# Performance work log

Hardware: AMD Instinct MI355X
Metric: run time of the kernel (lower is better)

## Reference

```python
import jax, jax.numpy as jnp
import numpy as np

EPS = 1e-5
DN = ('NCHW', 'OIHW', 'NCHW')

def _conv(x, w, b):
    y = jax.lax.conv_general_dilated(x, w, (1, 1), 'SAME', dimension_numbers=DN)
    return y + b.reshape(1, -1, 1, 1)

def _bn(x, g, bt, m, v):
    # inference-mode BatchNorm2d
    scale = g * jax.lax.rsqrt(v + EPS)
    return (x - m.reshape(1, -1, 1, 1)) * scale.reshape(1, -1, 1, 1) + bt.reshape(1, -1, 1, 1)


def setup_inputs() -> dict:
    key = jax.random.key(0)
    ks = jax.random.split(key, 12)
    B, C, H, W = 32, 1, 1024, 1024
    inp = {
        'x':  jax.random.normal(ks[0], (B, C, H, W), jnp.float32),
        # conv3x3_bn_r (shared module, used 3 times)
        'wa': jax.random.normal(ks[1], (1, 1, 3, 3), jnp.float32) * 0.2,
        'ba': jnp.zeros((1,), jnp.float32),
        'ga': jnp.ones((1,), jnp.float32),
        'bta': jnp.zeros((1,), jnp.float32),
        'ma': jax.random.normal(ks[2], (1,), jnp.float32) * 0.1,
        'va': jax.random.uniform(ks[3], (1,), jnp.float32) + 0.5,
        # conv3x3_bn
        'wb': jax.random.normal(ks[4], (1, 1, 3, 3), jnp.float32) * 0.2,
        'bb': jnp.zeros((1,), jnp.float32),
        'gb': jnp.ones((1,), jnp.float32),
        'btb': jnp.zeros((1,), jnp.float32),
        'mb': jax.random.normal(ks[5], (1,), jnp.float32) * 0.1,
        'vb': jax.random.uniform(ks[6], (1,), jnp.float32) + 0.5,
        # conv1x1_bn
        'wc': jax.random.normal(ks[7], (1, 1, 1, 1), jnp.float32) * 0.2,
        'bc': jnp.zeros((1,), jnp.float32),
        'gc': jnp.ones((1,), jnp.float32),
        'btc': jnp.zeros((1,), jnp.float32),
        'mc': jax.random.normal(ks[8], (1,), jnp.float32) * 0.1,
        'vc': jax.random.uniform(ks[9], (1,), jnp.float32) + 0.5,
        # conv3x3_r
        'wd': jax.random.normal(ks[10], (1, 1, 3, 3), jnp.float32) * 0.2,
        'bd': jnp.zeros((1,), jnp.float32),
        # conv1x1
        'we': jax.random.normal(ks[11], (1, 1, 1, 1), jnp.float32) * 0.2,
        'be': jnp.zeros((1,), jnp.float32),
    }
    return inp


def reference(x, wa, ba, ga, bta, ma, va, wb, bb, gb, btb, mb, vb,
              wc, bc, gc, btc, mc, vc, wd, bd, we, be):
    # t = 0 (top-left corner): right->left cummax + bottom->up cummax
    # conv3x3_bn_r is one shared module; x1 == x2 in the original.
    x1 = jax.nn.relu(_bn(_conv(x, wa, ba), ga, bta, ma, va))
    i1 = jax.lax.cummax(x1, axis=3, reverse=True)  # RightLeftMaxPooling
    i2 = jax.lax.cummax(x1, axis=2, reverse=True)  # DownUpMaxPooling
    b1 = _bn(_conv(i1 + i2, wb, bb), gb, btb, mb, vb)
    b2 = _bn(_conv(x, wc, bc), gc, btc, mc, vc)
    s = jax.nn.relu(b1 + b2)
    out = jax.nn.relu(_bn(_conv(s, wa, ba), ga, bta, ma, va))  # shared conv3x3_bn_r again
    out = jax.nn.relu(_conv(out, wd, bd))
    out = _conv(out, we, be)
    return out
```

## Files before the change

### kernel.cpp

```cpp
#include <hip/hip_runtime.h>
#include <math.h>

#define EPS 1e-5f
constexpr int IMG_H = 1024;
constexpr int IMG_W = 1024;
constexpr int NIMG  = 32;

__device__ __forceinline__ float frelu(float v) { return fmaxf(v, 0.f); }

struct Row { float4 q[4]; };

__device__ __forceinline__ void load_row(const float* __restrict__ xim, int gr,
                                         int lane, Row& R)
{
    if ((unsigned)gr < (unsigned)IMG_H) {
        const float4* rp = (const float4*)(xim + (size_t)gr * IMG_W);
#pragma unroll
        for (int q = 0; q < 4; ++q) R.q[q] = rp[lane + 64 * q];
    } else {
#pragma unroll
        for (int q = 0; q < 4; ++q) R.q[q] = make_float4(0.f, 0.f, 0.f, 0.f);
    }
}

__device__ __forceinline__ void conv3_row(const Row& Ra, const Row& Rb, const Row& Rc,
                                          const float* ws, float bias, int lane,
                                          float4* v)
{
    const Row* rows[3] = { &Ra, &Rb, &Rc };
#pragma unroll
    for (int q = 0; q < 4; ++q) {
        float acc0 = bias, acc1 = bias, acc2 = bias, acc3 = bias;
#pragma unroll
        for (int dy = 0; dy < 3; ++dy) {
            float4 C = rows[dy]->q[q];
            float Lw = __shfl_up(C.w, 1, 64);
            float Bq = 0.f;
            if (q > 0) Bq = __shfl(rows[dy]->q[q - 1].w, 63, 64);
            if (lane == 0) Lw = Bq;
            float Rx = __shfl_down(C.x, 1, 64);
            float Aq = 0.f;
            if (q < 3) Aq = __shfl(rows[dy]->q[q + 1].x, 0, 64);
            if (lane == 63) Rx = Aq;
            const float w0 = ws[3 * dy], w1 = ws[3 * dy + 1], w2 = ws[3 * dy + 2];
            acc0 += w0 * Lw  + w1 * C.x + w2 * C.y;
            acc1 += w0 * C.x + w1 * C.y + w2 * C.z;
            acc2 += w0 * C.y + w1 * C.z + w2 * C.w;
            acc3 += w0 * C.z + w1 * C.w + w2 * Rx;
        }
        v[q] = make_float4(frelu(acc0), frelu(acc1), frelu(acc2), frelu(acc3));
    }
}

__global__ __launch_bounds__(256) void k_rowstats(
    const float* __restrict__ x,
    const float* __restrict__ wa, const float* __restrict__ ba,
    const float* __restrict__ ga, const float* __restrict__ bta,
    const float* __restrict__ ma, const float* __restrict__ va,
    float* __restrict__ M8, float* __restrict__ I1S)
{
    const int bid  = blockIdx.x;
    const int img  = bid >> 6;
    const int b16  = bid & 63;
    const int lane = threadIdx.x & 63;
    const int wv   = threadIdx.x >> 6;
    const int rb   = b16 * 16 + wv * 4;

    const float scale = ga[0] * rsqrtf(va[0] + EPS);
    float w_s[9];
#pragma unroll
    for (int k = 0; k < 9; ++k) w_s[k] = wa[k] * scale;
    const float bias = (ba[0] - ma[0]) * scale + bta[0];

    const float* xim = x + (size_t)img * IMG_H * IMG_W;

    Row A, B, C;
    load_row(xim, rb - 1, lane, A);
    load_row(xim, rb,     lane, B);

    float4 cm[4];
#pragma unroll
    for (int q = 0; q < 4; ++q) cm[q] = make_float4(0.f, 0.f, 0.f, 0.f);

#pragma unroll
    for (int rr = 0; rr < 4; ++rr) {
        const int r = rb + rr;
        load_row(xim, r + 1, lane, C);
        float4 v[4];
        conv3_row(A, B, C, w_s, bias, lane, v);

        float4 s[4]; float T4[4], e[4];
#pragma unroll
        for (int q = 0; q < 4; ++q) {
            float s3 = v[q].w;
            float s2 = fmaxf(v[q].z, s3);
            float s1 = fmaxf(v[q].y, s2);
            float s0 = fmaxf(v[q].x, s1);
            s[q] = make_float4(s0, s1, s2, s3);
            float mm = s0;
#pragma unroll
            for (int off = 1; off < 64; off <<= 1) {
                float o = __shfl_down(mm, off, 64);
                if (lane + off < 64) mm = fmaxf(mm, o);
            }
            T4[q] = __shfl(mm, 0, 64);
            float ex = __shfl_down(mm, 1, 64);
            if (lane == 63) ex = -INFINITY;
            e[q] = ex;
        }
        float Rr[4];
        Rr[3] = -INFINITY;
        Rr[2] = T4[3];
        Rr[1] = fmaxf(T4[2], Rr[2]);
        Rr[0] = fmaxf(T4[1], Rr[1]);

        if ((lane & 15) == 0) {
#pragma unroll
            for (int q = 0; q < 4; ++q) {
                const float ee  = fmaxf(e[q], Rr[q]);
                const float i1w = fmaxf(s[q].w, ee);
                I1S[((size_t)img * IMG_H + r) * 16 + (q * 4 + (lane >> 4))] = i1w;
            }
        }
#pragma unroll
        for (int q = 0; q < 4; ++q) {
            cm[q].x = fmaxf(cm[q].x, v[q].x); cm[q].y = fmaxf(cm[q].y, v[q].y);
            cm[q].z = fmaxf(cm[q].z, v[q].z); cm[q].w = fmaxf(cm[q].w, v[q].w);
        }
        A = B; B = C;
    }

    __shared__ float4 wcm[4][256];
#pragma unroll
    for (int q = 0; q < 4; ++q) wcm[wv][64 * q + lane] = cm[q];
    __syncthreads();

    const int tid = threadIdx.x;
    float4 a0 = wcm[0][tid], a1 = wcm[1][tid];
    float4 a2 = wcm[2][tid], a3 = wcm[3][tid];
    float4 f0 = make_float4(fmaxf(a0.x, a1.x), fmaxf(a0.y, a1.y),
                            fmaxf(a0.z, a1.z), fmaxf(a0.w, a1.w));
    float4 f1 = make_float4(fmaxf(a2.x, a3.x), fmaxf(a2.y, a3.y),
                            fmaxf(a2.z, a3.z), fmaxf(a2.w, a3.w));
    const int s0 = b16 * 2;
    ((float4*)(M8 + ((size_t)img * 128 + s0) * IMG_W))[tid]     = f0;
    ((float4*)(M8 + ((size_t)img * 128 + s0 + 1) * IMG_W))[tid] = f1;
}

__global__ __launch_bounds__(256) void k_seed(
    const float* __restrict__ M8, float* __restrict__ I2S)
{
    const int gid = blockIdx.x * 256 + threadIdx.x;
    const int img = gid >> 10;
    const int c   = gid & 1023;
    const float* mp = M8  + (size_t)img * 128 * IMG_W + c;
    float*       ip = I2S + (size_t)img * 16  * IMG_W + c;

    float run = 0.f;
#pragma unroll 8
    for (int s = 127; s >= 8; --s) {
        if ((s & 7) == 0) ip[(size_t)(s / 8 - 1) * IMG_W] = run;
        run = fmaxf(run, mp[(size_t)s * IMG_W]);
    }
}

__global__ __launch_bounds__(256) void k_tile(
    const float* __restrict__ x,
    const float* __restrict__ I1S, const float* __restrict__ I2S,
    const float* __restrict__ wa, const float* __restrict__ ba,
    const float* __restrict__ ga, const float* __restrict__ bta,
    const float* __restrict__ ma, const float* __restrict__ va,
    const float* __restrict__ wb, const float* __restrict__ bb,
    const float* __restrict__ gb, const float* __restrict__ btb,
    const float* __restrict__ mb, const float* __restrict__ vb,
    const float* __restrict__ wc, const float* __restrict__ bc,
    const float* __restrict__ gcp, const float* __restrict__ btc,
    const float* __restrict__ mc, const float* __restrict__ vc,
    const float* __restrict__ wd, const float* __restrict__ bd,
    const float* __restrict__ we, const float* __restrict__ be,
    float* __restrict__ out)
{
    __shared__ float B1[75 * 72];
    __shared__ float B2[70 * 72];

    const int bid = blockIdx.x;
    const int img = bid >> 8;
    const int tr  = (bid >> 4) & 15;
    const int tc  = bid & 15;
    const int r0  = tr * 64, c0 = tc * 64;
    const int tid = threadIdx.x;
    const int k0  = tc + 1;
    const int m1  = tr;

    const float sa = ga[0] * rsqrtf(va[0] + EPS);
    float was[9];
#pragma unroll
    for (int k = 0; k < 9; ++k) was[k] = wa[k] * sa;
    const float biasa = (ba[0] - ma[0]) * sa + bta[0];

    const float sb = gb[0] * rsqrtf(vb[0] + EPS);
    float wbs[9];
#pragma unroll
    for (int k = 0; k < 9; ++k) wbs[k] = wb[k] * sb;
    const float biasb = (bb[0] - mb[0]) * sb + btb[0];

    const float sc = gcp[0] * rsqrtf(vc[0] + EPS);
    const float kc = wc[0] * sc;
    const float biasc = (bc[0] - mc[0]) * sc + btc[0];

    float wd9[9];
#pragma unroll
    for (int k = 0; k < 9; ++k) wd9[k] = wd[k];
    const float bd0 = bd[0], we0 = we[0], be0 = be[0];

    const float* xim = x + (size_t)img * IMG_H * IMG_W;

#pragma unroll
    for (int it = 0; it < 2; ++it) {
        const int m = tid + 256 * it;
        if (m < 270) {
            const int mi = m / 18, mj = m - mi * 18;
            const int wr0 = mi * 5, wc0 = mj * 4;
            const int gr0 = r0 + wr0 - 4;
            const int gc0 = c0 + wc0 - 4;
            const bool fastC = (gc0 >= 0) && (gc0 + 5 < IMG_W);
            float w[7][6];
#pragma unroll
            for (int rr = 0; rr < 7; ++rr) {
                const int gr = gr0 + rr;
                if ((unsigned)gr < (unsigned)IMG_H) {
                    const float* rp = xim + (size_t)gr * IMG_W;
                    if (fastC) {
                        float4 a4 = *(const float4*)(rp + gc0);
                        float2 b2 = *(const float2*)(rp + gc0 + 4);
                        w[rr][0] = a4.x; w[rr][1] = a4.y; w[rr][2] = a4.z;
                        w[rr][3] = a4.w; w[rr][4] = b2.x; w[rr][5] = b2.y;
                    } else {
#pragma unroll
                        for (int j = 0; j < 6; ++j) {
                            const int gc = gc0 + j;
                            w[rr][j] = ((unsigned)gc < (unsigned)IMG_W) ? rp[gc] : 0.f;
                        }
                    }
                } else {
#pragma unroll
                    for (int j = 0; j < 6; ++j) w[rr][j] = 0.f;
                }
            }
#pragma unroll
            for (int rr = 0; rr < 5; ++rr) {
                const int grx = r0 - 3 + wr0 + rr;
                float res4[4];
#pragma unroll
                for (int cc = 0; cc < 4; ++cc) {
                    float acc = biasa;
#pragma unroll
                    for (int dy = 0; dy < 3; ++dy)
#pragma unroll
                        for (int dx = 0; dx < 3; ++dx)
                            acc += was[3 * dy + dx] * w[rr + dy][cc + dx];
                    const int gcx = c0 - 3 + wc0 + cc;
                    float val = 0.f;
                    if ((unsigned)grx < (unsigned)IMG_H && (unsigned)gcx < (unsigned)IMG_W)
                        val = frelu(acc);
                    res4[cc] = val;
                }
                *(float4*)&B1[(wr0 + rr) * 72 + wc0] =
                    make_float4(res4[0], res4[1], res4[2], res4[3]);
            }
        }
    }
    __syncthreads();

    {
        const int wv = tid >> 6, lane = tid & 63;
#pragma unroll
        for (int k = 0; k < 18; ++k) {
            const int wr = k * 4 + wv;
            if (wr < 70) {
                const int row = r0 - 3 + wr;
                float seed = 0.f;
                if (k0 < 16 && (unsigned)row < (unsigned)IMG_H)
                    seed = I1S[((size_t)img * IMG_H + row) * 16 + k0];
                const float lo = B1[wr * 72 + lane];
                const float hi = (lane < 6) ? B1[wr * 72 + 64 + lane] : 0.f;
                float sh = hi;
#pragma unroll
                for (int off = 1; off < 64; off <<= 1) {
                    float o = __shfl_down(sh, off, 64);
                    if (lane + off < 64) sh = fmaxf(sh, o);
                }
                sh = fmaxf(sh, seed);
                const float hi_all = __shfl(sh, 0, 64);
                float sl = lo;
#pragma unroll
                for (int off = 1; off < 64; off <<= 1) {
                    float o = __shfl_down(sl, off, 64);
                    if (lane + off < 64) sl = fmaxf(sl, o);
                }
                B2[wr * 72 + lane] = fmaxf(sl, hi_all);
                if (lane < 6) B2[wr * 72 + 64 + lane] = sh;
            }
        }
    }
    __syncthreads();

    if (tid < 70) {
        const int col = c0 - 3 + tid;
        const bool colIn = (unsigned)col < (unsigned)IMG_W;
        float run = 0.f;
        if (m1 < 15 && colIn) run = I2S[((size_t)img * 16 + m1) * IMG_W + col];
#pragma unroll
        for (int wr = 74; wr >= 70; --wr) run = fmaxf(run, B1[wr * 72 + tid]);
#pragma unroll 7
        for (int wr = 69; wr >= 0; --wr) {
            run = fmaxf(run, B1[wr * 72 + tid]);
            const int r = r0 - 3 + wr;
            const bool inb = colIn && ((unsigned)r < (unsigned)IMG_H);
            const float tv = B2[wr * 72 + tid] + run;
            B2[wr * 72 + tid] = inb ? tv : 0.f;
        }
    }
    __syncthreads();

#pragma unroll
    for (int it = 0; it < 2; ++it) {
        const int m = tid + 256 * it;
        if (m < 289) {
            const int mi = m / 17, mj = m - mi * 17;
            const int si0 = mi * 4, sj0 = mj * 4;
            float win[6][6];
#pragma unroll
            for (int r = 0; r < 6; ++r) {
                const float* p = &B2[(si0 + r) * 72 + sj0];
                float4 a4 = *(const float4*)p;
                float2 b2 = *(const float2*)(p + 4);
                win[r][0] = a4.x; win[r][1] = a4.y; win[r][2] = a4.z;
                win[r][3] = a4.w; win[r][4] = b2.x; win[r][5] = b2.y;
            }
#pragma unroll
            for (int a = 0; a < 4; ++a) {
                float res4[4];
#pragma unroll
                for (int b = 0; b < 4; ++b) {
                    float acc = biasb;
#pragma unroll
                    for (int dy = 0; dy < 3; ++dy)
#pragma unroll
                        for (int dx = 0; dx < 3; ++dx)
                            acc += wbs[3 * dy + dx] * win[a + dy][b + dx];
                    const int gr = r0 - 2 + si0 + a, gc = c0 - 2 + sj0 + b;
                    float sres = 0.f;
                    if ((unsigned)gr < (unsigned)IMG_H && (unsigned)gc < (unsigned)IMG_W) {
                        const float xv = xim[(size_t)gr * IMG_W + gc];
                        sres = frelu(acc + xv * kc + biasc);
                    }
                    res4[b] = sres;
                }
                *(float4*)&B1[(si0 + a) * 72 + sj0] =
                    make_float4(res4[0], res4[1], res4[2], res4[3]);
            }
        }
    }
    __syncthreads();

#pragma unroll
    for (int it = 0; it < 2; ++it) {
        const int m = tid + 256 * it;
        if (m < 289) {
            const int mi = m / 17, mj = m - mi * 17;
            const int ai0 = mi * 4, aj0 = mj * 4;
            float win[6][6];
#pragma unroll
            for (int r = 0; r < 6; ++r) {
                const float* p = &B1[(ai0 + r) * 72 + aj0];
                float4 a4 = *(const float4*)p;
                float2 b2 = *(const float2*)(p + 4);
                win[r][0] = a4.x; win[r][1] = a4.y; win[r][2] = a4.z;
                win[r][3] = a4.w; win[r][4] = b2.x; win[r][5] = b2.y;
            }
#pragma unroll
            for (int a = 0; a < 4; ++a) {
                float res4[4];
#pragma unroll
                for (int b = 0; b < 4; ++b) {
                    float acc = biasa;
#pragma unroll
                    for (int dy = 0; dy < 3; ++dy)
#pragma unroll
                        for (int dx = 0; dx < 3; ++dx)
                            acc += was[3 * dy + dx] * win[a + dy][b + dx];
                    const int gr = r0 - 1 + ai0 + a, gc = c0 - 1 + aj0 + b;
                    float r1 = 0.f;
                    if ((unsigned)gr < (unsigned)IMG_H && (unsigned)gc < (unsigned)IMG_W)
                        r1 = frelu(acc);
                    res4[b] = r1;
                }
                *(float4*)&B2[(ai0 + a) * 72 + aj0] =
                    make_float4(res4[0], res4[1], res4[2], res4[3]);
            }
        }
    }
    __syncthreads();

    {
        const int oi0 = (tid >> 4) << 2, oj0 = (tid & 15) << 2;
        float win[6][6];
#pragma unroll
        for (int r = 0; r < 6; ++r) {
            const float* p = &B2[(oi0 + r) * 72 + oj0];
            float4 a4 = *(const float4*)p;
            float2 b2 = *(const float2*)(p + 4);
            win[r][0] = a4.x; win[r][1] = a4.y; win[r][2] = a4.z;
            win[r][3] = a4.w; win[r][4] = b2.x; win[r][5] = b2.y;
        }
        float* oim = out + (size_t)img * IMG_H * IMG_W;
#pragma unroll
        for (int a = 0; a < 4; ++a) {
            float res4[4];
#pragma unroll
            for (int b = 0; b < 4; ++b) {
                float acc = bd0;
#pragma unroll
                for (int dy = 0; dy < 3; ++dy)
#pragma unroll
                    for (int dx = 0; dx < 3; ++dx)
                        acc += wd9[3 * dy + dx] * win[a + dy][b + dx];
                res4[b] = frelu(acc) * we0 + be0;
            }
            *(float4*)&oim[(size_t)(r0 + oi0 + a) * IMG_W + (c0 + oj0)] =
                make_float4(res4[0], res4[1], res4[2], res4[3]);
        }
    }
}

extern "C" void kernel_launch(void* const* d_in, const int* in_sizes, int n_in,
                              void* d_out, int out_size, void* d_ws, size_t ws_size,
                              hipStream_t stream)
{
    const float* x   = (const float*)d_in[0];
    const float* wa  = (const float*)d_in[1];
    const float* ba  = (const float*)d_in[2];
    const float* ga  = (const float*)d_in[3];
    const float* bta = (const float*)d_in[4];
    const float* ma  = (const float*)d_in[5];
    const float* va  = (const float*)d_in[6];
    const float* wb  = (const float*)d_in[7];
    const float* bb  = (const float*)d_in[8];
    const float* gb  = (const float*)d_in[9];
    const float* btb = (const float*)d_in[10];
    const float* mb  = (const float*)d_in[11];
    const float* vb  = (const float*)d_in[12];
    const float* wc  = (const float*)d_in[13];
    const float* bc  = (const float*)d_in[14];
    const float* gcp = (const float*)d_in[15];
    const float* btc = (const float*)d_in[16];
    const float* mc  = (const float*)d_in[17];
    const float* vc  = (const float*)d_in[18];
    const float* wd  = (const float*)d_in[19];
    const float* bd  = (const float*)d_in[20];
    const float* we  = (const float*)d_in[21];
    const float* be  = (const float*)d_in[22];

    float* outp = (float*)d_out;
    float* M8   = (float*)d_ws;
    float* I1S  = M8 + (size_t)NIMG * 128 * IMG_W;
    float* I2S  = I1S + (size_t)NIMG * IMG_H * 16;

    k_rowstats<<<dim3(NIMG * 64), dim3(256), 0, stream>>>(
        x, wa, ba, ga, bta, ma, va, M8, I1S);
    k_seed<<<dim3(128), dim3(256), 0, stream>>>(M8, I2S);
    k_tile<<<dim3(NIMG * 256), dim3(256), 0, stream>>>(
        x, I1S, I2S, wa, ba, ga, bta, ma, va, wb, bb, gb, btb, mb, vb,
        wc, bc, gcp, btc, mc, vc, wd, bd, we, be, outp);
}
```

Baseline: 576.1 us.

## Shrink tile halo, restructure seeds and scans across front and tile kernels

The main tile kernel drops from 64x64 tiles with a 5-row bottom halo to 64x32 tiles with a smaller halo. Seeds are made finer: I1S now holds 32 column seeds per row and I2S is built from M8 plus new partial maxima (M8part). The front kernel processes 2 rows per wave in 8-row strips instead of 4 rows per wave, so it launches twice as many blocks. The column cummax in the tile becomes a per-wave partial max followed by a merged row loop, replacing the separate single-wave scan pass. This trims redundant halo convolution and LDS traffic and raises occupancy, at the cost of more blocks, more seed traffic and more halo overhead relative to the narrower tile width.

Result: faster. 511.9 us (-11.1%).

```diff
diff --git a/kernel.cpp b/kernel.cpp
--- a/kernel.cpp
+++ b/kernel.cpp
@@ -8,63 +8,19 @@
 
 __device__ __forceinline__ float frelu(float v) { return fmaxf(v, 0.f); }
 
-struct Row { float4 q[4]; };
-
-__device__ __forceinline__ void load_row(const float* __restrict__ xim, int gr,
-                                         int lane, Row& R)
-{
-    if ((unsigned)gr < (unsigned)IMG_H) {
-        const float4* rp = (const float4*)(xim + (size_t)gr * IMG_W);
-#pragma unroll
-        for (int q = 0; q < 4; ++q) R.q[q] = rp[lane + 64 * q];
-    } else {
-#pragma unroll
-        for (int q = 0; q < 4; ++q) R.q[q] = make_float4(0.f, 0.f, 0.f, 0.f);
-    }
-}
-
-__device__ __forceinline__ void conv3_row(const Row& Ra, const Row& Rb, const Row& Rc,
-                                          const float* ws, float bias, int lane,
-                                          float4* v)
-{
-    const Row* rows[3] = { &Ra, &Rb, &Rc };
-#pragma unroll
-    for (int q = 0; q < 4; ++q) {
-        float acc0 = bias, acc1 = bias, acc2 = bias, acc3 = bias;
-#pragma unroll
-        for (int dy = 0; dy < 3; ++dy) {
-            float4 C = rows[dy]->q[q];
-            float Lw = __shfl_up(C.w, 1, 64);
-            float Bq = 0.f;
-            if (q > 0) Bq = __shfl(rows[dy]->q[q - 1].w, 63, 64);
-            if (lane == 0) Lw = Bq;
-            float Rx = __shfl_down(C.x, 1, 64);
-            float Aq = 0.f;
-            if (q < 3) Aq = __shfl(rows[dy]->q[q + 1].x, 0, 64);
-            if (lane == 63) Rx = Aq;
-            const float w0 = ws[3 * dy], w1 = ws[3 * dy + 1], w2 = ws[3 * dy + 2];
-            acc0 += w0 * Lw  + w1 * C.x + w2 * C.y;
-            acc1 += w0 * C.x + w1 * C.y + w2 * C.z;
-            acc2 += w0 * C.y + w1 * C.z + w2 * C.w;
-            acc3 += w0 * C.z + w1 * C.w + w2 * Rx;
-        }
-        v[q] = make_float4(frelu(acc0), frelu(acc1), frelu(acc2), frelu(acc3));
-    }
-}
-
-__global__ __launch_bounds__(256) void k_rowstats(
+__global__ __launch_bounds__(256) void k_front(
     const float* __restrict__ x,
     const float* __restrict__ wa, const float* __restrict__ ba,
     const float* __restrict__ ga, const float* __restrict__ bta,
     const float* __restrict__ ma, const float* __restrict__ va,
-    float* __restrict__ M8, float* __restrict__ I1S)
+    float* __restrict__ M8, float* __restrict__ M8part, float* __restrict__ I1S)
 {
-    const int bid  = blockIdx.x;
-    const int img  = bid >> 6;
-    const int b16  = bid & 63;
-    const int lane = threadIdx.x & 63;
-    const int wv   = threadIdx.x >> 6;
-    const int rb   = b16 * 16 + wv * 4;
+    const int bid   = blockIdx.x;
+    const int img   = bid >> 7;
+    const int strip = bid & 127;
+    const int lane  = threadIdx.x & 63;
+    const int wv    = threadIdx.x >> 6;
+    const int rb    = strip * 8 + wv * 2;
 
     const float scale = ga[0] * rsqrtf(va[0] + EPS);
     float w_s[9];
@@ -74,29 +30,55 @@
 
     const float* xim = x + (size_t)img * IMG_H * IMG_W;
 
-    Row A, B, C;
-    load_row(xim, rb - 1, lane, A);
-    load_row(xim, rb,     lane, B);
-
-    float4 cm[4];
-#pragma unroll
-    for (int q = 0; q < 4; ++q) cm[q] = make_float4(0.f, 0.f, 0.f, 0.f);
-
-#pragma unroll
-    for (int rr = 0; rr < 4; ++rr) {
-        const int r = rb + rr;
-        load_row(xim, r + 1, lane, C);
+    float4 X[4][4];
+#pragma unroll
+    for (int ri = 0; ri < 4; ++ri) {
+        const int gr = rb - 1 + ri;
+        if (gr >= 0 && gr < IMG_H) {
+            const float4* rp = (const float4*)(xim + (size_t)gr * IMG_W);
+#pragma unroll
+            for (int q = 0; q < 4; ++q) X[ri][q] = rp[lane + 64 * q];
+        } else {
+#pragma unroll
+            for (int q = 0; q < 4; ++q) X[ri][q] = make_float4(0.f, 0.f, 0.f, 0.f);
+        }
+    }
+
+    float4 wm[4], w1r1[4];
+#pragma unroll
+    for (int rr = 0; rr < 2; ++rr) {
         float4 v[4];
-        conv3_row(A, B, C, w_s, bias, lane, v);
-
-        float4 s[4]; float T4[4], e[4];
+#pragma unroll
+        for (int q = 0; q < 4; ++q) {
+            float acc0 = bias, acc1 = bias, acc2 = bias, acc3 = bias;
+#pragma unroll
+            for (int dy = 0; dy < 3; ++dy) {
+                float4 C = X[rr + dy][q];
+                float Lw = __shfl_up(C.w, 1, 64);
+                float Bq = 0.f;
+                if (q > 0) Bq = __shfl(X[rr + dy][q - 1].w, 63, 64);
+                if (lane == 0) Lw = Bq;
+                float Rx = __shfl_down(C.x, 1, 64);
+                float Aq = 0.f;
+                if (q < 3) Aq = __shfl(X[rr + dy][q + 1].x, 0, 64);
+                if (lane == 63) Rx = Aq;
+                const float w0 = w_s[3 * dy], w1 = w_s[3 * dy + 1], w2 = w_s[3 * dy + 2];
+                acc0 += w0 * Lw  + w1 * C.x + w2 * C.y;
+                acc1 += w0 * C.x + w1 * C.y + w2 * C.z;
+                acc2 += w0 * C.y + w1 * C.z + w2 * C.w;
+                acc3 += w0 * C.z + w1 * C.w + w2 * Rx;
+            }
+            v[q] = make_float4(frelu(acc0), frelu(acc1), frelu(acc2), frelu(acc3));
+        }
+
+        float sW[4], T4[4], e[4];
 #pragma unroll
         for (int q = 0; q < 4; ++q) {
             float s3 = v[q].w;
             float s2 = fmaxf(v[q].z, s3);
             float s1 = fmaxf(v[q].y, s2);
             float s0 = fmaxf(v[q].x, s1);
-            s[q] = make_float4(s0, s1, s2, s3);
+            sW[q] = s3;
             float mm = s0;
 #pragma unroll
             for (int off = 1; off < 64; off <<= 1) {
@@ -114,57 +96,81 @@
         Rr[1] = fmaxf(T4[2], Rr[2]);
         Rr[0] = fmaxf(T4[1], Rr[1]);
 
-        if ((lane & 15) == 0) {
+        if ((lane & 7) == 0) {
+            const int r = rb + rr;
 #pragma unroll
             for (int q = 0; q < 4; ++q) {
-                const float ee  = fmaxf(e[q], Rr[q]);
-                const float i1w = fmaxf(s[q].w, ee);
-                I1S[((size_t)img * IMG_H + r) * 16 + (q * 4 + (lane >> 4))] = i1w;
-            }
-        }
-#pragma unroll
-        for (int q = 0; q < 4; ++q) {
-            cm[q].x = fmaxf(cm[q].x, v[q].x); cm[q].y = fmaxf(cm[q].y, v[q].y);
-            cm[q].z = fmaxf(cm[q].z, v[q].z); cm[q].w = fmaxf(cm[q].w, v[q].w);
-        }
-        A = B; B = C;
-    }
-
-    __shared__ float4 wcm[4][256];
-#pragma unroll
-    for (int q = 0; q < 4; ++q) wcm[wv][64 * q + lane] = cm[q];
+                const float val = fmaxf(sW[q], fmaxf(e[q], Rr[q]));
+                I1S[((size_t)img * IMG_H + r) * 32 + (q * 8 + (lane >> 3))] = val;
+            }
+        }
+
+        if (rr == 0) {
+#pragma unroll
+            for (int q = 0; q < 4; ++q) wm[q] = v[q];
+        } else {
+#pragma unroll
+            for (int q = 0; q < 4; ++q) {
+                wm[q].x = fmaxf(wm[q].x, v[q].x); wm[q].y = fmaxf(wm[q].y, v[q].y);
+                wm[q].z = fmaxf(wm[q].z, v[q].z); wm[q].w = fmaxf(wm[q].w, v[q].w);
+            }
+#pragma unroll
+            for (int q = 0; q < 4; ++q) w1r1[q] = v[q];
+        }
+    }
+
+    __shared__ float4 wmax[5][256];
+#pragma unroll
+    for (int q = 0; q < 4; ++q) wmax[wv][64 * q + lane] = wm[q];
+    if (wv == 1) {
+#pragma unroll
+        for (int q = 0; q < 4; ++q) wmax[4][64 * q + lane] = w1r1[q];
+    }
     __syncthreads();
 
     const int tid = threadIdx.x;
-    float4 a0 = wcm[0][tid], a1 = wcm[1][tid];
-    float4 a2 = wcm[2][tid], a3 = wcm[3][tid];
-    float4 f0 = make_float4(fmaxf(a0.x, a1.x), fmaxf(a0.y, a1.y),
-                            fmaxf(a0.z, a1.z), fmaxf(a0.w, a1.w));
-    float4 f1 = make_float4(fmaxf(a2.x, a3.x), fmaxf(a2.y, a3.y),
-                            fmaxf(a2.z, a3.z), fmaxf(a2.w, a3.w));
-    const int s0 = b16 * 2;
-    ((float4*)(M8 + ((size_t)img * 128 + s0) * IMG_W))[tid]     = f0;
-    ((float4*)(M8 + ((size_t)img * 128 + s0 + 1) * IMG_W))[tid] = f1;
+    float4 a0 = wmax[0][tid], a1 = wmax[1][tid], a2 = wmax[2][tid], a3 = wmax[3][tid];
+    float4 f;
+    f.x = fmaxf(fmaxf(a0.x, a1.x), fmaxf(a2.x, a3.x));
+    f.y = fmaxf(fmaxf(a0.y, a1.y), fmaxf(a2.y, a3.y));
+    f.z = fmaxf(fmaxf(a0.z, a1.z), fmaxf(a2.z, a3.z));
+    f.w = fmaxf(fmaxf(a0.w, a1.w), fmaxf(a2.w, a3.w));
+    ((float4*)(M8 + ((size_t)img * 128 + strip) * IMG_W))[tid] = f;
+
+    if (strip >= 8 && (strip & 7) == 0) {
+        float4 r3v = wmax[4][tid];
+        float4 fp;
+        fp.x = fmaxf(r3v.x, fmaxf(a2.x, a3.x));
+        fp.y = fmaxf(r3v.y, fmaxf(a2.y, a3.y));
+        fp.z = fmaxf(r3v.z, fmaxf(a2.z, a3.z));
+        fp.w = fmaxf(r3v.w, fmaxf(a2.w, a3.w));
+        ((float4*)(M8part + ((size_t)img * 15 + ((strip >> 3) - 1)) * IMG_W))[tid] = fp;
+    }
 }
 
-__global__ __launch_bounds__(256) void k_seed(
-    const float* __restrict__ M8, float* __restrict__ I2S)
+__global__ __launch_bounds__(256) void k_seed2(
+    const float* __restrict__ M8, const float* __restrict__ M8part,
+    float* __restrict__ I2S)
 {
     const int gid = blockIdx.x * 256 + threadIdx.x;
     const int img = gid >> 10;
     const int c   = gid & 1023;
-    const float* mp = M8  + (size_t)img * 128 * IMG_W + c;
-    float*       ip = I2S + (size_t)img * 16  * IMG_W + c;
+    const float* mp = M8 + (size_t)img * 128 * IMG_W + c;
 
     float run = 0.f;
-#pragma unroll 8
-    for (int s = 127; s >= 8; --s) {
-        if ((s & 7) == 0) ip[(size_t)(s / 8 - 1) * IMG_W] = run;
+#pragma unroll 7
+    for (int s = 127; s >= 9; --s) {
         run = fmaxf(run, mp[(size_t)s * IMG_W]);
+        if ((s & 7) == 1) {
+            const int m = (s - 9) >> 3;
+            const size_t o = ((size_t)img * 15 + m) * IMG_W + c;
+            I2S[o] = fmaxf(run, M8part[o]);
+        }
     }
 }
 
-__global__ __launch_bounds__(256) void k_tile(
+#define PITCH 44
+__global__ __launch_bounds__(256, 6) void k_tile(
     const float* __restrict__ x,
     const float* __restrict__ I1S, const float* __restrict__ I2S,
     const float* __restrict__ wa, const float* __restrict__ ba,
@@ -180,17 +186,35 @@
     const float* __restrict__ we, const float* __restrict__ be,
     float* __restrict__ out)
 {
-    __shared__ float B1[75 * 72];
-    __shared__ float B2[70 * 72];
+    __shared__ float B1[70 * PITCH];
+    __shared__ float B2[68 * PITCH];
+    __shared__ float P[4][PITCH];
 
     const int bid = blockIdx.x;
-    const int img = bid >> 8;
-    const int tr  = (bid >> 4) & 15;
-    const int tc  = bid & 15;
-    const int r0  = tr * 64, c0 = tc * 64;
+    const int img = bid >> 9;
+    const int tr  = (bid >> 5) & 15;
+    const int tc  = bid & 31;
+    const int r0  = tr * 64, c0 = tc * 32;
     const int tid = threadIdx.x;
-    const int k0  = tc + 1;
-    const int m1  = tr;
+    const int lane = tid & 63;
+    const int wv   = tid >> 6;
+
+    const float* xim = x + (size_t)img * IMG_H * IMG_W;
+
+    float i2sv = 0.f;
+    if (tr < 15 && lane < 38) {
+        const int col = c0 - 3 + lane;
+        if ((unsigned)col < (unsigned)IMG_W)
+            i2sv = I2S[((size_t)img * 15 + tr) * IMG_W + col];
+    }
+    const int g0 = wv * 18;
+    const int nrows = (wv == 3) ? 16 : 18;
+    float seed1v = 0.f;
+    if (lane < nrows && tc < 31) {
+        const int row = r0 - 3 + g0 + lane;
+        if ((unsigned)row < (unsigned)IMG_H)
+            seed1v = I1S[((size_t)img * IMG_H + row) * 32 + (tc + 1)];
+    }
 
     const float sa = ga[0] * rsqrtf(va[0] + EPS);
     float was[9];
@@ -213,42 +237,38 @@
     for (int k = 0; k < 9; ++k) wd9[k] = wd[k];
     const float bd0 = bd[0], we0 = we[0], be0 = be[0];
 
-    const float* xim = x + (size_t)img * IMG_H * IMG_W;
-
-#pragma unroll
-    for (int it = 0; it < 2; ++it) {
-        const int m = tid + 256 * it;
-        if (m < 270) {
-            const int mi = m / 18, mj = m - mi * 18;
-            const int wr0 = mi * 5, wc0 = mj * 4;
-            const int gr0 = r0 + wr0 - 4;
-            const int gc0 = c0 + wc0 - 4;
-            const bool fastC = (gc0 >= 0) && (gc0 + 5 < IMG_W);
-            float w[7][6];
-#pragma unroll
-            for (int rr = 0; rr < 7; ++rr) {
-                const int gr = gr0 + rr;
-                if ((unsigned)gr < (unsigned)IMG_H) {
-                    const float* rp = xim + (size_t)gr * IMG_W;
-                    if (fastC) {
-                        float4 a4 = *(const float4*)(rp + gc0);
-                        float2 b2 = *(const float2*)(rp + gc0 + 4);
-                        w[rr][0] = a4.x; w[rr][1] = a4.y; w[rr][2] = a4.z;
-                        w[rr][3] = a4.w; w[rr][4] = b2.x; w[rr][5] = b2.y;
-                    } else {
-#pragma unroll
-                        for (int j = 0; j < 6; ++j) {
-                            const int gc = gc0 + j;
-                            w[rr][j] = ((unsigned)gc < (unsigned)IMG_W) ? rp[gc] : 0.f;
-                        }
+    if (tid < 180) {
+        const int mi = tid / 10, mj = tid - mi * 10;
+        const int wr0 = mi * 4, wc0 = mj * 4;
+        const int gr0 = r0 - 4 + wr0;
+        const int gc0 = c0 - 4 + wc0;
+        const bool fastC = (gc0 >= 0) && (gc0 + 5 < IMG_W);
+        float w[6][6];
+#pragma unroll
+        for (int rr = 0; rr < 6; ++rr) {
+            const int gr = gr0 + rr;
+            if ((unsigned)gr < (unsigned)IMG_H) {
+                const float* rp = xim + (size_t)gr * IMG_W;
+                if (fastC) {
+                    float4 a4 = *(const float4*)(rp + gc0);
+                    float2 b2 = *(const float2*)(rp + gc0 + 4);
+                    w[rr][0] = a4.x; w[rr][1] = a4.y; w[rr][2] = a4.z;
+                    w[rr][3] = a4.w; w[rr][4] = b2.x; w[rr][5] = b2.y;
+                } else {
+#pragma unroll
+                    for (int j = 0; j < 6; ++j) {
+                        const int gc = gc0 + j;
+                        w[rr][j] = ((unsigned)gc < (unsigned)IMG_W) ? rp[gc] : 0.f;
                     }
-                } else {
-#pragma unroll
-                    for (int j = 0; j < 6; ++j) w[rr][j] = 0.f;
                 }
-            }
-#pragma unroll
-            for (int rr = 0; rr < 5; ++rr) {
+            } else {
+#pragma unroll
+                for (int j = 0; j < 6; ++j) w[rr][j] = 0.f;
+            }
+        }
+#pragma unroll
+        for (int rr = 0; rr < 4; ++rr) {
+            if (wr0 + rr < 70) {
                 const int grx = r0 - 3 + wr0 + rr;
                 float res4[4];
 #pragma unroll
@@ -265,7 +285,7 @@
                         val = frelu(acc);
                     res4[cc] = val;
                 }
-                *(float4*)&B1[(wr0 + rr) * 72 + wc0] =
+                *(float4*)&B1[(wr0 + rr) * PITCH + wc0] =
                     make_float4(res4[0], res4[1], res4[2], res4[3]);
             }
         }
@@ -273,114 +293,99 @@
     __syncthreads();
 
     {
-        const int wv = tid >> 6, lane = tid & 63;
-#pragma unroll
+        float pm = 0.f;
+        if (lane < 38) {
+            for (int k = 0; k < nrows; ++k)
+                pm = fmaxf(pm, B1[(g0 + k) * PITCH + lane]);
+            P[wv][lane] = pm;
+        }
+    }
+    __syncthreads();
+
+    {
+        float run = i2sv;
+#pragma unroll
+        for (int w2 = 1; w2 < 4; ++w2)
+            if (w2 > wv && lane < 38) run = fmaxf(run, P[w2][lane]);
+#pragma unroll 6
         for (int k = 0; k < 18; ++k) {
-            const int wr = k * 4 + wv;
-            if (wr < 70) {
+            if (k < nrows) {
+                const int lr = nrows - 1 - k;
+                const int wr = g0 + lr;
+                const float xv = (lane < 38) ? B1[wr * PITCH + lane] : 0.f;
+                float mm = xv;
+#pragma unroll
+                for (int off = 1; off < 64; off <<= 1) {
+                    float o = __shfl_down(mm, off, 64);
+                    if (lane + off < 64) mm = fmaxf(mm, o);
+                }
+                const float sd = __shfl(seed1v, lr, 64);
+                const float i1v = fmaxf(mm, sd);
+                run = fmaxf(run, xv);
                 const int row = r0 - 3 + wr;
-                float seed = 0.f;
-                if (k0 < 16 && (unsigned)row < (unsigned)IMG_H)
-                    seed = I1S[((size_t)img * IMG_H + row) * 16 + k0];
-                const float lo = B1[wr * 72 + lane];
-                const float hi = (lane < 6) ? B1[wr * 72 + 64 + lane] : 0.f;
-                float sh = hi;
-#pragma unroll
-                for (int off = 1; off < 64; off <<= 1) {
-                    float o = __shfl_down(sh, off, 64);
-                    if (lane + off < 64) sh = fmaxf(sh, o);
+                const int col = c0 - 3 + lane;
+                const bool inb = ((unsigned)row < (unsigned)IMG_H) &&
+                                 ((unsigned)col < (unsigned)IMG_W);
+                if (lane < 38)
+                    B1[wr * PITCH + lane] = inb ? (i1v + run) : 0.f;
+            }
+        }
+    }
+    __syncthreads();
+
+    if (tid < 153) {
+        const int mi = tid / 9, mj = tid - mi * 9;
+        const int si0 = mi * 4, sj0 = mj * 4;
+        float win[6][6];
+#pragma unroll
+        for (int r = 0; r < 6; ++r) {
+            const float* p = &B1[(si0 + r) * PITCH + sj0];
+            float4 a4 = *(const float4*)p;
+            float2 b2 = *(const float2*)(p + 4);
+            win[r][0] = a4.x; win[r][1] = a4.y; win[r][2] = a4.z;
+            win[r][3] = a4.w; win[r][4] = b2.x; win[r][5] = b2.y;
+        }
+#pragma unroll
+        for (int a = 0; a < 4; ++a) {
+            float res4[4];
+#pragma unroll
+            for (int b = 0; b < 4; ++b) {
+                float acc = biasb;
+#pragma unroll
+                for (int dy = 0; dy < 3; ++dy)
+#pragma unroll
+                    for (int dx = 0; dx < 3; ++dx)
+                        acc += wbs[3 * dy + dx] * win[a + dy][b + dx];
+                const int gr = r0 - 2 + si0 + a, gc = c0 - 2 + sj0 + b;
+                float sres = 0.f;
+                if ((unsigned)gr < (unsigned)IMG_H && (unsigned)gc < (unsigned)IMG_W) {
+                    const float xv = xim[(size_t)gr * IMG_W + gc];
+                    sres = frelu(acc + xv * kc + biasc);
                 }
-                sh = fmaxf(sh, seed);
-                const float hi_all = __shfl(sh, 0, 64);
-                float sl = lo;
-#pragma unroll
-                for (int off = 1; off < 64; off <<= 1) {
-                    float o = __shfl_down(sl, off, 64);
-                    if (lane + off < 64) sl = fmaxf(sl, o);
-                }
-                B2[wr * 72 + lane] = fmaxf(sl, hi_all);
-                if (lane < 6) B2[wr * 72 + 64 + lane] = sh;
-            }
-        }
-    }
-    __syncthreads();
-
-    if (tid < 70) {
-        const int col = c0 - 3 + tid;
-        const bool colIn = (unsigned)col < (unsigned)IMG_W;
-        float run = 0.f;
-        if (m1 < 15 && colIn) run = I2S[((size_t)img * 16 + m1) * IMG_W + col];
-#pragma unroll
-        for (int wr = 74; wr >= 70; --wr) run = fmaxf(run, B1[wr * 72 + tid]);
-#pragma unroll 7
-        for (int wr = 69; wr >= 0; --wr) {
-            run = fmaxf(run, B1[wr * 72 + tid]);
-            const int r = r0 - 3 + wr;
-            const bool inb = colIn && ((unsigned)r < (unsigned)IMG_H);
-            const float tv = B2[wr * 72 + tid] + run;
-            B2[wr * 72 + tid] = inb ? tv : 0.f;
-        }
-    }
-    __syncthreads();
-
-#pragma unroll
-    for (int it = 0; it < 2; ++it) {
-        const int m = tid + 256 * it;
-        if (m < 289) {
-            const int mi = m / 17, mj = m - mi * 17;
-            const int si0 = mi * 4, sj0 = mj * 4;
-            float win[6][6];
-#pragma unroll
-            for (int r = 0; r < 6; ++r) {
-                const float* p = &B2[(si0 + r) * 72 + sj0];
-                float4 a4 = *(const float4*)p;
-                float2 b2 = *(const float2*)(p + 4);
-                win[r][0] = a4.x; win[r][1] = a4.y; win[r][2] = a4.z;
-                win[r][3] = a4.w; win[r][4] = b2.x; win[r][5] = b2.y;
-            }
-#pragma unroll
-            for (int a = 0; a < 4; ++a) {
-                float res4[4];
-#pragma unroll
-                for (int b = 0; b < 4; ++b) {
-                    float acc = biasb;
-#pragma unroll
-                    for (int dy = 0; dy < 3; ++dy)
-#pragma unroll
-                        for (int dx = 0; dx < 3; ++dx)
-                            acc += wbs[3 * dy + dx] * win[a + dy][b + dx];
-                    const int gr = r0 - 2 + si0 + a, gc = c0 - 2 + sj0 + b;
-                    float sres = 0.f;
-                    if ((unsigned)gr < (unsigned)IMG_H && (unsigned)gc < (unsigned)IMG_W) {
-                        const float xv = xim[(size_t)gr * IMG_W + gc];
-                        sres = frelu(acc + xv * kc + biasc);
-                    }
-                    res4[b] = sres;
-                }
-                *(float4*)&B1[(si0 + a) * 72 + sj0] =
-                    make_float4(res4[0], res4[1], res4[2], res4[3]);
-            }
-        }
-    }
-    __syncthreads();
-
-#pragma unroll
-    for (int it = 0; it < 2; ++it) {
-        const int m = tid + 256 * it;
-        if (m < 289) {
-            const int mi = m / 17, mj = m - mi * 17;
-            const int ai0 = mi * 4, aj0 = mj * 4;
-            float win[6][6];
-#pragma unroll
-            for (int r = 0; r < 6; ++r) {
-                const float* p = &B1[(ai0 + r) * 72 + aj0];
-                float4 a4 = *(const float4*)p;
-                float2 b2 = *(const float2*)(p + 4);
-                win[r][0] = a4.x; win[r][1] = a4.y; win[r][2] = a4.z;
-                win[r][3] = a4.w; win[r][4] = b2.x; win[r][5] = b2.y;
-            }
-#pragma unroll
-            for (int a = 0; a < 4; ++a) {
+                res4[b] = sres;
+            }
+            *(float4*)&B2[(si0 + a) * PITCH + sj0] =
+                make_float4(res4[0], res4[1], res4[2], res4[3]);
+        }
+    }
+    __syncthreads();
+
+    if (tid < 153) {
+        const int mi = tid / 9, mj = tid - mi * 9;
+        const int ai0 = mi * 4, aj0 = mj * 4;
+        float win[6][6];
+#pragma unroll
+        for (int r = 0; r < 6; ++r) {
+            const int rrow = (ai0 + r < 68) ? (ai0 + r) : 67;
+            const float* p = &B2[rrow * PITCH + aj0];
+            float4 a4 = *(const float4*)p;
+            float2 b2 = *(const float2*)(p + 4);
+            win[r][0] = a4.x; win[r][1] = a4.y; win[r][2] = a4.z;
+            win[r][3] = a4.w; win[r][4] = b2.x; win[r][5] = b2.y;
+        }
+#pragma unroll
+        for (int a = 0; a < 4; ++a) {
+            if (ai0 + a < 66) {
                 float res4[4];
 #pragma unroll
                 for (int b = 0; b < 4; ++b) {
@@ -396,7 +401,7 @@
                         r1 = frelu(acc);
                     res4[b] = r1;
                 }
-                *(float4*)&B2[(ai0 + a) * 72 + aj0] =
+                *(float4*)&B1[(ai0 + a) * PITCH + aj0] =
                     make_float4(res4[0], res4[1], res4[2], res4[3]);
             }
         }
@@ -404,11 +409,11 @@
     __syncthreads();
 
     {
-        const int oi0 = (tid >> 4) << 2, oj0 = (tid & 15) << 2;
-        float win[6][6];
-#pragma unroll
-        for (int r = 0; r < 6; ++r) {
-            const float* p = &B2[(oi0 + r) * 72 + oj0];
+        const int oi0 = (tid >> 3) * 2, oj0 = (tid & 7) * 4;
+        float win[4][6];
+#pragma unroll
+        for (int r = 0; r < 4; ++r) {
+            const float* p = &B1[(oi0 + r) * PITCH + oj0];
             float4 a4 = *(const float4*)p;
             float2 b2 = *(const float2*)(p + 4);
             win[r][0] = a4.x; win[r][1] = a4.y; win[r][2] = a4.z;
@@ -416,7 +421,7 @@
         }
         float* oim = out + (size_t)img * IMG_H * IMG_W;
 #pragma unroll
-        for (int a = 0; a < 4; ++a) {
+        for (int a = 0; a < 2; ++a) {
             float res4[4];
 #pragma unroll
             for (int b = 0; b < 4; ++b) {
@@ -462,15 +467,16 @@
     const float* we  = (const float*)d_in[21];
     const float* be  = (const float*)d_in[22];
 
-    float* outp = (float*)d_out;
-    float* M8   = (float*)d_ws;
-    float* I1S  = M8 + (size_t)NIMG * 128 * IMG_W;
-    float* I2S  = I1S + (size_t)NIMG * IMG_H * 16;
-
-    k_rowstats<<<dim3(NIMG * 64), dim3(256), 0, stream>>>(
-        x, wa, ba, ga, bta, ma, va, M8, I1S);
-    k_seed<<<dim3(128), dim3(256), 0, stream>>>(M8, I2S);
-    k_tile<<<dim3(NIMG * 256), dim3(256), 0, stream>>>(
+    float* outp   = (float*)d_out;
+    float* M8     = (float*)d_ws;
+    float* M8part = M8 + (size_t)NIMG * 128 * IMG_W;
+    float* I1S    = M8part + (size_t)NIMG * 15 * IMG_W;
+    float* I2S    = I1S + (size_t)NIMG * IMG_H * 32;
+
+    k_front<<<dim3(NIMG * 128), dim3(256), 0, stream>>>(
+        x, wa, ba, ga, bta, ma, va, M8, M8part, I1S);
+    k_seed2<<<dim3(128), dim3(256), 0, stream>>>(M8, M8part, I2S);
+    k_tile<<<dim3(NIMG * 16 * 32), dim3(256), 0, stream>>>(
         x, I1S, I2S, wa, ba, ga, bta, ma, va, wb, bb, gb, btb, mb, vb,
         wc, bc, gcp, btc, mc, vc, wd, bd, we, be, outp);
 }
```
